# Kernel optimization log

Hardware: AMD Instinct MI355X
Metric: run time of the kernel (lower is better)

## Reference

```python
import jax, jax.numpy as jnp
import numpy as np

N = 100000
E = 1600000
DIN = 128
H = 64
OUT_CLAMP = 10.0


def setup_inputs() -> dict:
    key = jax.random.key(0)
    ks = jax.random.split(key, 8)
    x = jax.random.normal(ks[0], (N, DIN), dtype=jnp.float32)
    edge_index = jax.random.randint(ks[1], (2, E), 0, N, dtype=jnp.int64)
    edge_weight = jax.random.uniform(ks[2], (E,), dtype=jnp.float32)
    # learned params (glorot-ish scale)
    W1 = jax.random.normal(ks[3], (DIN, H), dtype=jnp.float32) / np.sqrt(DIN)
    b1 = jnp.zeros((H,), dtype=jnp.float32)
    W2 = jax.random.normal(ks[4], (H, H), dtype=jnp.float32) / np.sqrt(H)
    b2 = jnp.zeros((H,), dtype=jnp.float32)
    fc_w = jax.random.normal(ks[5], (H, 1), dtype=jnp.float32) / np.sqrt(H)
    fc_b = jnp.zeros((1,), dtype=jnp.float32)
    return {"x": x, "edge_index": edge_index, "edge_weight": edge_weight,
            "W1": W1, "b1": b1, "W2": W2, "b2": b2, "fc_w": fc_w, "fc_b": fc_b}


def _gcn_conv(h, src, dst, norm, W, b, n_nodes):
    # h: [N, Fin] -> [N, Fout]. PyG GCNConv: linear, gather at source,
    # scale by symmetric norm, scatter-add at target, add bias.
    hw = h @ W                                   # [N, Fout]
    msg = hw[src] * norm[:, None]                # [E+N, Fout]
    out = jax.ops.segment_sum(msg, dst, num_segments=n_nodes)
    return out + b


def _gcn_norm(edge_index, edge_weight, n_nodes):
    # add self-loops with weight 1, compute deg^-1/2 symmetric norm
    loop = jnp.arange(n_nodes, dtype=edge_index.dtype)
    src = jnp.concatenate([edge_index[0], loop])
    dst = jnp.concatenate([edge_index[1], loop])
    ew = jnp.concatenate([edge_weight, jnp.ones((n_nodes,), edge_weight.dtype)])
    deg = jax.ops.segment_sum(ew, dst, num_segments=n_nodes)
    dis = jnp.where(deg > 0, jax.lax.rsqrt(jnp.maximum(deg, 1e-12)), 0.0)
    norm = dis[src] * ew * dis[dst]
    return src, dst, norm


def reference(x, edge_index, edge_weight, W1, b1, W2, b2, fc_w, fc_b):
    src, dst, norm = _gcn_norm(edge_index, edge_weight, N)
    h = _gcn_conv(x, src, dst, norm, W1, b1, N)
    h = _gcn_conv(h, src, dst, norm, W2, b2, N)
    out = h @ fc_w + fc_b                        # [N, 1]
    out = jnp.clip(out, 0.0, OUT_CLAMP)
    return jnp.round(out)
```

## Files before the change

kernel.cpp:

```cpp
#include <hip/hip_runtime.h>

#define DIN 128
#define BINW 128
#define BINSHIFT 7
#define NB_MAX 1024
#define CHUNK 8192


__global__ void precompute_kernel(const float* __restrict__ W1, const float* __restrict__ b1,
                                  const float* __restrict__ W2, const float* __restrict__ b2,
                                  const float* __restrict__ fcw, const float* __restrict__ fcb,
                                  double* __restrict__ w1f, double* __restrict__ cvals) {
    const int t = threadIdx.x;
    __shared__ double sw2f[64];
    if (t < 64) {
        double s = 0.0;
        for (int j = 0; j < 64; j++) s += (double)W2[t * 64 + j] * (double)fcw[j];
        sw2f[t] = s;
    }
    __syncthreads();
    if (t < 128) {
        double s = 0.0;
        for (int j = 0; j < 64; j++) s += (double)W1[t * 64 + j] * sw2f[j];
        w1f[t] = s;
    }
    if (t == 128) {
        double c1 = 0.0, c0 = (double)fcb[0];
        for (int j = 0; j < 64; j++) {
            c1 += (double)b1[j] * sw2f[j];
            c0 += (double)b2[j] * (double)fcw[j];
        }
        cvals[0] = c0;
        cvals[1] = c1;
    }
}

__global__ __launch_bounds__(256) void hist_gemv_kernel(
        const int* __restrict__ dst, const float* __restrict__ X,
        const double* __restrict__ w1f, unsigned* __restrict__ histT,
        double* __restrict__ q, int n, int e, int nb, int hblk) {
    __shared__ unsigned cnt[NB_MAX];
    const int blk = blockIdx.x;
    const int t = threadIdx.x;
    if (blk < hblk) {
        for (int b = t; b < nb; b += 256) cnt[b] = 0u;
        __syncthreads();
        const long base = (long)blk * CHUNK;
        for (int k = 0; k < CHUNK / 256; k++) {
            long i = base + k * 256 + t;
            if (i < e) atomicAdd(&cnt[dst[i] >> BINSHIFT], 1u);
        }
        __syncthreads();
        for (int b = t; b < nb; b += 256)
            histT[(long)blk * nb + b] = cnt[b];
        return;
    }
    long g = (long)(blk - hblk) * 256 + t;
    int row = (int)(g >> 6);
    int lane = (int)(g & 63);
    if (row >= n) return;
    float2 x = *(const float2*)(X + (long)row * DIN + 2 * lane);
    double v = (double)x.x * w1f[2 * lane] + (double)x.y * w1f[2 * lane + 1];
#pragma unroll
    for (int off = 32; off > 0; off >>= 1) v += __shfl_down(v, off, 64);
    if (lane == 0) q[row] = v;
}

__global__ __launch_bounds__(256) void binscan_kernel(
        const unsigned* __restrict__ histT, unsigned* __restrict__ chunkOfsT,
        unsigned* __restrict__ binCnt, int nb, int hblk) {
    int gw = (int)((blockIdx.x * 256 + threadIdx.x) >> 6);
    int l = threadIdx.x & 63;
    if (gw >= nb) return;
    unsigned carry = 0u;
    for (int c0 = 0; c0 < hblk; c0 += 64) {
        int c = c0 + l;
        unsigned v = (c < hblk) ? histT[(long)c * nb + gw] : 0u;
        unsigned s = v;
#pragma unroll
        for (int off = 1; off < 64; off <<= 1) {
            unsigned u = __shfl_up(s, off, 64);
            if (l >= off) s += u;
        }
        if (c < hblk) chunkOfsT[(long)c * nb + gw] = carry + s - v;
        carry += (unsigned)__shfl((int)s, 63, 64);
    }
    if (l == 0) binCnt[gw] = carry;
}

__global__ void scan_kernel(const unsigned* __restrict__ binCnt,
                            unsigned* __restrict__ binBase, int nb) {
    __shared__ unsigned part[256];
    const int t = threadIdx.x;
    unsigned loc[4];
    unsigned s = 0;
#pragma unroll
    for (int k = 0; k < 4; k++) {
        int idx = t * 4 + k;
        unsigned v = (idx < nb) ? binCnt[idx] : 0u;
        loc[k] = s;
        s += v;
    }
    part[t] = s;
    __syncthreads();
    if (t == 0) {
        unsigned run = 0;
        for (int j = 0; j < 256; j++) { unsigned v = part[j]; part[j] = run; run += v; }
    }
    __syncthreads();
    unsigned p = part[t];
#pragma unroll
    for (int k = 0; k < 4; k++) {
        int idx = t * 4 + k;
        if (idx < nb) binBase[idx] = p + loc[k];
    }
    if (t == 255) binBase[nb] = p + s;
}

__global__ __launch_bounds__(1024) void binscatter_kernel(
        const int* __restrict__ src, const int* __restrict__ dst,
        const float* __restrict__ ew, const unsigned* __restrict__ binBase,
        const unsigned* __restrict__ chunkOfsT,
        uint2* __restrict__ binned, int e, int nb) {
    __shared__ unsigned cnt[NB_MAX];
    __shared__ unsigned sbase[NB_MAX];
    const int c = blockIdx.x;
    const int t = threadIdx.x;
    for (int b = t; b < nb; b += 1024) {
        cnt[b] = 0u;
        sbase[b] = binBase[b] + chunkOfsT[(long)c * nb + b];
    }
    __syncthreads();
    const long base = (long)c * CHUNK;
#pragma unroll
    for (int k = 0; k < CHUNK / 1024; k++) {
        long i = base + k * 1024 + t;
        if (i < e) {
            int d = dst[i];
            int b = d >> BINSHIFT;
            unsigned p = sbase[b] + atomicAdd(&cnt[b], 1u);
            binned[p] = uint2{(unsigned)src[i] | ((unsigned)(d & (BINW - 1)) << 20),
                              __float_as_uint(ew[i])};
        }
    }
}

__global__ __launch_bounds__(256) void setup_kernel(
        const uint2* __restrict__ binned, const unsigned* __restrict__ binBase,
        const double* __restrict__ cvals, const double* __restrict__ q,
        float* __restrict__ disA, double* __restrict__ v1,
        double* __restrict__ tpart, int n) {
    __shared__ float ws[BINW];
    const int b = blockIdx.x;
    const int t = threadIdx.x;
    if (t < BINW) ws[t] = 0.0f;
    __syncthreads();
    const unsigned s0 = binBase[b], s1 = binBase[b + 1];
    for (unsigned i = s0 + t; i < s1; i += 256) {
        uint2 v = binned[i];
        atomicAdd(&ws[v.x >> 20], __uint_as_float(v.y));
    }
    __syncthreads();
    if (t < BINW) {
        int node = b * BINW + t;
        if (node < n) {
            float d = 1.0f + ws[t];
            float di = (d > 0.0f) ? (1.0f / sqrtf(fmaxf(d, 1e-12f))) : 0.0f;
            double qv = q[node];
            disA[node] = di;
            v1[node] = (double)di * qv;
            tpart[node] = cvals[1] + (double)(di * di) * qv;
        }
    }
}

__global__ __launch_bounds__(256) void spmv1_kernel(
        const uint2* __restrict__ binned, const unsigned* __restrict__ binBase,
        const double* __restrict__ v1, const float* __restrict__ disA,
        const double* __restrict__ tpart, double* __restrict__ v2, int n) {
    __shared__ double acc[BINW];
    const int b = blockIdx.x;
    const int t = threadIdx.x;
    if (t < BINW) acc[t] = 0.0;
    __syncthreads();
    const unsigned s0 = binBase[b], s1 = binBase[b + 1];
    for (unsigned tile = s0; tile < s1; tile += 2048) {
        uint2 ee[8];
        double vv[8];
        bool ok[8];
#pragma unroll
        for (int k = 0; k < 8; k++) {
            unsigned idx = tile + t + k * 256u;
            ok[k] = (idx < s1);
            if (ok[k]) ee[k] = binned[idx];
        }
#pragma unroll
        for (int k = 0; k < 8; k++)
            if (ok[k]) vv[k] = v1[ee[k].x & 0xFFFFFu];
#pragma unroll
        for (int k = 0; k < 8; k++)
            if (ok[k])
                atomicAdd(&acc[ee[k].x >> 20],
                          (double)__uint_as_float(ee[k].y) * vv[k]);
    }
    __syncthreads();
    if (t < BINW) {
        int node = b * BINW + t;
        if (node < n) {
            double di = (double)disA[node];
            double tv = tpart[node] + di * acc[t];
            v2[node] = di * tv;
        }
    }
}

__global__ __launch_bounds__(256) void spmv2_head_kernel(
        const uint2* __restrict__ binned, const unsigned* __restrict__ binBase,
        const double* __restrict__ v2, const float* __restrict__ disA,
        const double* __restrict__ cvals, float* __restrict__ out, int n) {
    __shared__ double acc[BINW];
    const int b = blockIdx.x;
    const int t = threadIdx.x;
    if (t < BINW) acc[t] = 0.0;
    __syncthreads();
    const unsigned s0 = binBase[b], s1 = binBase[b + 1];
    for (unsigned tile = s0; tile < s1; tile += 2048) {
        uint2 ee[8];
        double vv[8];
        bool ok[8];
#pragma unroll
        for (int k = 0; k < 8; k++) {
            unsigned idx = tile + t + k * 256u;
            ok[k] = (idx < s1);
            if (ok[k]) ee[k] = binned[idx];
        }
#pragma unroll
        for (int k = 0; k < 8; k++)
            if (ok[k]) vv[k] = v2[ee[k].x & 0xFFFFFu];
#pragma unroll
        for (int k = 0; k < 8; k++)
            if (ok[k])
                atomicAdd(&acc[ee[k].x >> 20],
                          (double)__uint_as_float(ee[k].y) * vv[k]);
    }
    __syncthreads();
    if (t < BINW) {
        int node = b * BINW + t;
        if (node < n) {
            double u = cvals[0] + (double)disA[node] * (v2[node] + acc[t]);
            float o = (float)u;
            o = fminf(fmaxf(o, 0.0f), 10.0f);
            out[node] = rintf(o);
        }
    }
}

extern "C" void kernel_launch(void* const* d_in, const int* in_sizes, int n_in,
                              void* d_out, int out_size, void* d_ws, size_t ws_size,
                              hipStream_t stream) {
    const float* x   = (const float*)d_in[0];
    const int*   eix = (const int*)d_in[1];
    const float* ew  = (const float*)d_in[2];
    const float* W1  = (const float*)d_in[3];
    const float* b1  = (const float*)d_in[4];
    const float* W2  = (const float*)d_in[5];
    const float* b2  = (const float*)d_in[6];
    const float* fcw = (const float*)d_in[7];
    const float* fcb = (const float*)d_in[8];
    float* out = (float*)d_out;

    const int n = in_sizes[0] / DIN;
    const int e = in_sizes[2];
    const int* src = eix;
    const int* dst = eix + e;
    const int nb = (n + BINW - 1) / BINW;
    const int hblk = (e + CHUNK - 1) / CHUNK;

    auto al = [](size_t v) { return (v + 63) & ~(size_t)63; };
    double* ws = (double*)d_ws;
    size_t o = 0;
    double*   w1f     = ws + o; o += al(DIN);
    double*   cvals   = ws + o; o += al(2);
    double*   q       = ws + o; o += al((size_t)n);
    double*   tpart   = ws + o; o += al((size_t)n);
    double*   v1      = ws + o; o += al((size_t)n);
    double*   v2      = ws + o; o += al((size_t)n);
    float*    disA    = (float*)(ws + o);    o += al(((size_t)n + 1) / 2);
    unsigned* binCnt  = (unsigned*)(ws + o); o += al(((size_t)nb + 1) / 2);
    unsigned* binBase = (unsigned*)(ws + o); o += al(((size_t)nb + 2) / 2);
    unsigned* histT   = (unsigned*)(ws + o); o += al(((size_t)nb * hblk + 1) / 2);
    unsigned* chunkOfsT = (unsigned*)(ws + o); o += al(((size_t)nb * hblk + 1) / 2);
    uint2*    binned  = (uint2*)(ws + o);

    const int gemvblk = (n + 3) / 4;
    const int bsblk = (nb * 64 + 255) / 256;

    precompute_kernel<<<1, 256, 0, stream>>>(W1, b1, W2, b2, fcw, fcb, w1f, cvals);
    hist_gemv_kernel<<<hblk + gemvblk, 256, 0, stream>>>(dst, x, w1f, histT,
                                                         q, n, e, nb, hblk);
    binscan_kernel<<<bsblk, 256, 0, stream>>>(histT, chunkOfsT, binCnt, nb, hblk);
    scan_kernel<<<1, 256, 0, stream>>>(binCnt, binBase, nb);
    binscatter_kernel<<<hblk, 1024, 0, stream>>>(src, dst, ew, binBase, chunkOfsT,
                                                 binned, e, nb);
    setup_kernel<<<nb, 256, 0, stream>>>(binned, binBase, cvals, q, disA, v1,
                                         tpart, n);
    spmv1_kernel<<<nb, 256, 0, stream>>>(binned, binBase, v1, disA, tpart, v2, n);
    spmv2_head_kernel<<<nb, 256, 0, stream>>>(binned, binBase, v2, disA, cvals,
                                              out, n);
}
```

Measured before the change: 191.1 us.

## Vectorize edge loads, pack two GEMV rows per wave, privatize SpMV accumulators

The histogram and bin-scatter kernels now read dst/src/weight with 128-bit int4/float4 loads, handling four edges per thread and keeping a scalar tail path. The GEMV packs two rows per 64-lane wave using float4 loads, which halves the block count. Both SpMV kernels move to 512 threads with four private LDS accumulator copies per bin, reducing contention on the double-precision shared atomics, and sum the copies at the end. These changes target load instruction count and LDS atomic serialization, at the cost of more LDS per block and a different floating-point summation order.

```diff
diff --git a/kernel.cpp b/kernel.cpp
--- a/kernel.cpp
+++ b/kernel.cpp
@@ -46,9 +46,19 @@
         for (int b = t; b < nb; b += 256) cnt[b] = 0u;
         __syncthreads();
         const long base = (long)blk * CHUNK;
-        for (int k = 0; k < CHUNK / 256; k++) {
-            long i = base + k * 256 + t;
-            if (i < e) atomicAdd(&cnt[dst[i] >> BINSHIFT], 1u);
+#pragma unroll
+        for (int k = 0; k < CHUNK / 1024; k++) {
+            long i = base + ((long)k * 256 + t) * 4;
+            if (i + 3 < e) {
+                int4 d4 = *(const int4*)(dst + i);
+                atomicAdd(&cnt[d4.x >> BINSHIFT], 1u);
+                atomicAdd(&cnt[d4.y >> BINSHIFT], 1u);
+                atomicAdd(&cnt[d4.z >> BINSHIFT], 1u);
+                atomicAdd(&cnt[d4.w >> BINSHIFT], 1u);
+            } else {
+                for (int j = 0; j < 4; j++)
+                    if (i + j < e) atomicAdd(&cnt[dst[i + j] >> BINSHIFT], 1u);
+            }
         }
         __syncthreads();
         for (int b = t; b < nb; b += 256)
@@ -56,14 +66,18 @@
         return;
     }
     long g = (long)(blk - hblk) * 256 + t;
-    int row = (int)(g >> 6);
+    int w = (int)(g >> 6);
     int lane = (int)(g & 63);
+    int sub = lane >> 5;
+    int l = lane & 31;
+    int row = w * 2 + sub;
     if (row >= n) return;
-    float2 x = *(const float2*)(X + (long)row * DIN + 2 * lane);
-    double v = (double)x.x * w1f[2 * lane] + (double)x.y * w1f[2 * lane + 1];
-#pragma unroll
-    for (int off = 32; off > 0; off >>= 1) v += __shfl_down(v, off, 64);
-    if (lane == 0) q[row] = v;
+    float4 x = *(const float4*)(X + (long)row * DIN + 4 * l);
+    double v = (double)x.x * w1f[4 * l] + (double)x.y * w1f[4 * l + 1]
+             + (double)x.z * w1f[4 * l + 2] + (double)x.w * w1f[4 * l + 3];
+#pragma unroll
+    for (int off = 16; off > 0; off >>= 1) v += __shfl_down(v, off, 64);
+    if (l == 0) q[row] = v;
 }
 
 __global__ __launch_bounds__(256) void binscan_kernel(
@@ -133,14 +147,33 @@
     __syncthreads();
     const long base = (long)c * CHUNK;
 #pragma unroll
-    for (int k = 0; k < CHUNK / 1024; k++) {
-        long i = base + k * 1024 + t;
-        if (i < e) {
-            int d = dst[i];
-            int b = d >> BINSHIFT;
-            unsigned p = sbase[b] + atomicAdd(&cnt[b], 1u);
-            binned[p] = uint2{(unsigned)src[i] | ((unsigned)(d & (BINW - 1)) << 20),
-                              __float_as_uint(ew[i])};
+    for (int k = 0; k < CHUNK / 4096; k++) {
+        long i = base + ((long)k * 1024 + t) * 4;
+        if (i + 3 < e) {
+            int4 d4 = *(const int4*)(dst + i);
+            int4 s4 = *(const int4*)(src + i);
+            float4 w4 = *(const float4*)(ew + i);
+            int dd[4] = {d4.x, d4.y, d4.z, d4.w};
+            int ss[4] = {s4.x, s4.y, s4.z, s4.w};
+            float ww[4] = {w4.x, w4.y, w4.z, w4.w};
+#pragma unroll
+            for (int j = 0; j < 4; j++) {
+                int b = dd[j] >> BINSHIFT;
+                unsigned p = sbase[b] + atomicAdd(&cnt[b], 1u);
+                binned[p] = uint2{(unsigned)ss[j] | ((unsigned)(dd[j] & (BINW - 1)) << 20),
+                                  __float_as_uint(ww[j])};
+            }
+        } else {
+            for (int j = 0; j < 4; j++) {
+                long i2 = i + j;
+                if (i2 < e) {
+                    int d = dst[i2];
+                    int b = d >> BINSHIFT;
+                    unsigned p = sbase[b] + atomicAdd(&cnt[b], 1u);
+                    binned[p] = uint2{(unsigned)src[i2] | ((unsigned)(d & (BINW - 1)) << 20),
+                                      __float_as_uint(ew[i2])};
+                }
+            }
         }
     }
 }
@@ -174,80 +207,89 @@
     }
 }
 
-__global__ __launch_bounds__(256) void spmv1_kernel(
+__global__ __launch_bounds__(512) void spmv1_kernel(
         const uint2* __restrict__ binned, const unsigned* __restrict__ binBase,
         const double* __restrict__ v1, const float* __restrict__ disA,
         const double* __restrict__ tpart, double* __restrict__ v2, int n) {
-    __shared__ double acc[BINW];
+    __shared__ double acc[4][BINW];
     const int b = blockIdx.x;
     const int t = threadIdx.x;
-    if (t < BINW) acc[t] = 0.0;
+    const int sub = t >> 7;
+    {
+        double* f = &acc[0][0];
+        if (t < 512) f[t] = 0.0;
+    }
     __syncthreads();
     const unsigned s0 = binBase[b], s1 = binBase[b + 1];
     for (unsigned tile = s0; tile < s1; tile += 2048) {
-        uint2 ee[8];
-        double vv[8];
-        bool ok[8];
-#pragma unroll
-        for (int k = 0; k < 8; k++) {
-            unsigned idx = tile + t + k * 256u;
+        uint2 ee[4];
+        double vv[4];
+        bool ok[4];
+#pragma unroll
+        for (int k = 0; k < 4; k++) {
+            unsigned idx = tile + t + k * 512u;
             ok[k] = (idx < s1);
             if (ok[k]) ee[k] = binned[idx];
         }
 #pragma unroll
-        for (int k = 0; k < 8; k++)
+        for (int k = 0; k < 4; k++)
             if (ok[k]) vv[k] = v1[ee[k].x & 0xFFFFFu];
 #pragma unroll
-        for (int k = 0; k < 8; k++)
+        for (int k = 0; k < 4; k++)
             if (ok[k])
-                atomicAdd(&acc[ee[k].x >> 20],
+                atomicAdd(&acc[sub][ee[k].x >> 20],
                           (double)__uint_as_float(ee[k].y) * vv[k]);
     }
     __syncthreads();
     if (t < BINW) {
         int node = b * BINW + t;
         if (node < n) {
+            double S = acc[0][t] + acc[1][t] + acc[2][t] + acc[3][t];
             double di = (double)disA[node];
-            double tv = tpart[node] + di * acc[t];
-            v2[node] = di * tv;
-        }
-    }
-}
-
-__global__ __launch_bounds__(256) void spmv2_head_kernel(
+            v2[node] = di * (tpart[node] + di * S);
+        }
+    }
+}
+
+__global__ __launch_bounds__(512) void spmv2_head_kernel(
         const uint2* __restrict__ binned, const unsigned* __restrict__ binBase,
         const double* __restrict__ v2, const float* __restrict__ disA,
         const double* __restrict__ cvals, float* __restrict__ out, int n) {
-    __shared__ double acc[BINW];
+    __shared__ double acc[4][BINW];
     const int b = blockIdx.x;
     const int t = threadIdx.x;
-    if (t < BINW) acc[t] = 0.0;
+    const int sub = t >> 7;
+    {
+        double* f = &acc[0][0];
+        if (t < 512) f[t] = 0.0;
+    }
     __syncthreads();
     const unsigned s0 = binBase[b], s1 = binBase[b + 1];
     for (unsigned tile = s0; tile < s1; tile += 2048) {
-        uint2 ee[8];
-        double vv[8];
-        bool ok[8];
-#pragma unroll
-        for (int k = 0; k < 8; k++) {
-            unsigned idx = tile + t + k * 256u;
+        uint2 ee[4];
+        double vv[4];
+        bool ok[4];
+#pragma unroll
+        for (int k = 0; k < 4; k++) {
+            unsigned idx = tile + t + k * 512u;
             ok[k] = (idx < s1);
             if (ok[k]) ee[k] = binned[idx];
         }
 #pragma unroll
-        for (int k = 0; k < 8; k++)
+        for (int k = 0; k < 4; k++)
             if (ok[k]) vv[k] = v2[ee[k].x & 0xFFFFFu];
 #pragma unroll
-        for (int k = 0; k < 8; k++)
+        for (int k = 0; k < 4; k++)
             if (ok[k])
-                atomicAdd(&acc[ee[k].x >> 20],
+                atomicAdd(&acc[sub][ee[k].x >> 20],
                           (double)__uint_as_float(ee[k].y) * vv[k]);
     }
     __syncthreads();
     if (t < BINW) {
         int node = b * BINW + t;
         if (node < n) {
-            double u = cvals[0] + (double)disA[node] * (v2[node] + acc[t]);
+            double S = acc[0][t] + acc[1][t] + acc[2][t] + acc[3][t];
+            double u = cvals[0] + (double)disA[node] * (v2[node] + S);
             float o = (float)u;
             o = fminf(fmaxf(o, 0.0f), 10.0f);
             out[node] = rintf(o);
@@ -292,7 +334,7 @@
     unsigned* chunkOfsT = (unsigned*)(ws + o); o += al(((size_t)nb * hblk + 1) / 2);
     uint2*    binned  = (uint2*)(ws + o);
 
-    const int gemvblk = (n + 3) / 4;
+    const int gemvblk = (n + 7) / 8;
     const int bsblk = (nb * 64 + 255) / 256;
 
     precompute_kernel<<<1, 256, 0, stream>>>(W1, b1, W2, b2, fcw, fcb, w1f, cvals);
@@ -304,7 +346,7 @@
                                                  binned, e, nb);
     setup_kernel<<<nb, 256, 0, stream>>>(binned, binBase, cvals, q, disA, v1,
                                          tpart, n);
-    spmv1_kernel<<<nb, 256, 0, stream>>>(binned, binBase, v1, disA, tpart, v2, n);
-    spmv2_head_kernel<<<nb, 256, 0, stream>>>(binned, binBase, v2, disA, cvals,
+    spmv1_kernel<<<nb, 512, 0, stream>>>(binned, binBase, v1, disA, tpart, v2, n);
+    spmv2_head_kernel<<<nb, 512, 0, stream>>>(binned, binBase, v2, disA, cvals,
                                               out, n);
 }
```

New measurement: 173.9 us (median of 2 runs). 1.1x faster.
